# Optimization experiments

Measured on AMD Instinct MI355X. Metric: run time of the kernel, lower is better.

The kernel has to match this reference:

```python
import jax, jax.numpy as jnp
import numpy as np

N_ENTITIES = 100000
N_RELATIONS = 1000
EMBED_DIM = 256
BATCH = 1024


def setup_inputs() -> dict:
    key = jax.random.key(0)
    k1, k2, k3 = jax.random.split(key, 3)
    queries = jax.random.randint(k1, (BATCH, 3), 0, N_RELATIONS, dtype=jnp.int64)
    entity_emb = jax.random.normal(k2, (N_ENTITIES, EMBED_DIM), dtype=jnp.float32)
    relation_emb = jax.random.normal(k3, (N_RELATIONS, EMBED_DIM), dtype=jnp.float32)
    return {"queries": queries, "entity_emb": entity_emb, "relation_emb": relation_emb}


def reference(queries, entity_emb, relation_emb):
    """Score every entity as the tail of each (head, relation, ?) query.

    Original torch code loops over entities computing
      -||E[head] + R[rel] - E[tail]||^2
    per tail. We collapse this into one GEMM via the expansion
      ||hr - E||^2 = ||hr||^2 - 2 hr.E^T + ||E||^2.
    """
    heads = queries[:, 0]
    rels = queries[:, 1]
    hr = entity_emb[heads] + relation_emb[rels]          # [B, D]
    hr_sq = jnp.sum(hr * hr, axis=-1, keepdims=True)      # [B, 1]
    ent_sq = jnp.sum(entity_emb * entity_emb, axis=-1)    # [N]
    cross = jnp.einsum("bd,nd->bn", hr, entity_emb)      # [B, N]
    scores = -(hr_sq - 2.0 * cross + ent_sq[None, :])     # [B, N]
    predictions = jnp.argmax(scores, axis=-1)             # [B]
    return scores, predictions
```

## Files before the change

kernel.cpp:

```cpp
#include <hip/hip_runtime.h>

#define MM 1024
#define NE 100000
#define KD 256
#define NT 782
#define NTILE 1563
#define PSTRIDE 784

typedef __attribute__((ext_vector_type(8))) short bf16x8;
typedef __attribute__((ext_vector_type(4))) float f32x4;
typedef __attribute__((ext_vector_type(4))) short short4v;

#define WS_HRSQ   524288
#define WS_ENTSQ  528384
#define WS_PART   1048576
#define WS_ENTB   8388608
#define WS_NEED   (WS_ENTB + (size_t)NE * KD * 2)

#define AS1 __attribute__((address_space(1)))
#define AS3 __attribute__((address_space(3)))

__device__ __forceinline__ void gld_lds16(const void* g, void* l) {
    __builtin_amdgcn_global_load_lds((const AS1 unsigned int*)g,
                                     (AS3 unsigned int*)l, 16, 0, 0);
}

__device__ __forceinline__ unsigned short f2bf(float f) {
    union { float f; unsigned int u; } v; v.f = f;
    unsigned int u = v.u;
    return (unsigned short)((u + 0x7FFFu + ((u >> 16) & 1u)) >> 16);
}

__device__ __forceinline__ bf16x8 pack8(float4 a, float4 b) {
    bf16x8 t;
    t[0] = (short)f2bf(a.x); t[1] = (short)f2bf(a.y);
    t[2] = (short)f2bf(a.z); t[3] = (short)f2bf(a.w);
    t[4] = (short)f2bf(b.x); t[5] = (short)f2bf(b.y);
    t[6] = (short)f2bf(b.z); t[7] = (short)f2bf(b.w);
    return t;
}

__device__ __forceinline__ unsigned long long packkey(float s, int col) {
    unsigned int u = __float_as_uint(s);
    unsigned int key = u ^ ((unsigned int)((int)u >> 31) | 0x80000000u);
    return ((unsigned long long)key << 32) | (unsigned int)(~col);
}

__global__ __launch_bounds__(64) void prep_kernel(const int* __restrict__ q,
                                                  const float* __restrict__ ent,
                                                  const float* __restrict__ rel,
                                                  unsigned short* __restrict__ hrb,
                                                  float* __restrict__ hrsq) {
    int b = blockIdx.x;
    int lane = threadIdx.x;
    int head = q[b * 3 + 0];
    int r    = q[b * 3 + 1];
    float4 e  = ((const float4*)(ent + (size_t)head * KD))[lane];
    float4 rv = ((const float4*)(rel + (size_t)r * KD))[lane];
    float4 h; h.x = e.x + rv.x; h.y = e.y + rv.y; h.z = e.z + rv.z; h.w = e.w + rv.w;
    short4v hv;
    hv[0] = (short)f2bf(h.x); hv[1] = (short)f2bf(h.y);
    hv[2] = (short)f2bf(h.z); hv[3] = (short)f2bf(h.w);
    *(short4v*)(hrb + (size_t)b * KD + lane * 4) = hv;
    float sq = h.x * h.x + h.y * h.y + h.z * h.z + h.w * h.w;
    #pragma unroll
    for (int off = 32; off > 0; off >>= 1) sq += __shfl_down(sq, off, 64);
    if (lane == 0) hrsq[b] = sq;
}

__global__ __launch_bounds__(256) void conv_entsq_kernel(const float* __restrict__ ent,
                                                         unsigned short* __restrict__ entb,
                                                         float* __restrict__ entsq) {
    int gw   = (blockIdx.x * 256 + threadIdx.x) >> 6;
    int lane = threadIdx.x & 63;
    int row  = gw * 2 + (lane >> 5);
    if (row >= NE) return;
    const float4* src = (const float4*)(ent + (size_t)row * KD) + (lane & 31) * 2;
    float4 a = src[0], b = src[1];
    *(bf16x8*)(entb + (size_t)row * KD + (lane & 31) * 8) = pack8(a, b);
    float s = a.x * a.x + a.y * a.y + a.z * a.z + a.w * a.w
            + b.x * b.x + b.y * b.y + b.z * b.z + b.w * b.w;
    #pragma unroll
    for (int off = 16; off > 0; off >>= 1) s += __shfl_xor(s, off, 64);
    if ((lane & 31) == 0) entsq[row] = s;
}

__global__ __launch_bounds__(256) void entsq_kernel(const float* __restrict__ ent,
                                                    float* __restrict__ entsq) {
    int w = threadIdx.x >> 6, lane = threadIdx.x & 63;
    int n = blockIdx.x * 4 + w;
    if (n >= NE) return;
    float4 v = ((const float4*)(ent + (size_t)n * KD))[lane];
    float s = v.x * v.x + v.y * v.y + v.z * v.z + v.w * v.w;
    #pragma unroll
    for (int off = 32; off > 0; off >>= 1) s += __shfl_down(s, off, 64);
    if (lane == 0) entsq[n] = s;
}

__global__ __launch_bounds__(256, 2) void gemm_v14(const unsigned short* __restrict__ hrb,
                                                   const unsigned short* __restrict__ entb,
                                                   const float* __restrict__ hrsq,
                                                   const float* __restrict__ entsq,
                                                   float* __restrict__ out,
                                                   unsigned long long* __restrict__ part) {
    __shared__ __align__(16) char SMEM[65536];

    const int bid    = blockIdx.x;
    const int qpanel = bid >> 6;
    const int g      = bid & 63;
    const int q0     = qpanel * 128;

    const int tid  = threadIdx.x;
    const int lane = tid & 63;
    const int wid  = tid >> 6;
    const int lr = lane & 15;
    const int lg = lane >> 4;
    const int qw = q0 + wid * 32;

    const int nT = (NTILE - g + 63) >> 6;

    float hq[2]; unsigned qoff[2];
    #pragma unroll
    for (int nn = 0; nn < 2; ++nn) {
        int qq = qw + nn * 16 + lr;
        hq[nn] = hrsq[qq];
        qoff[nn] = (unsigned)qq * (unsigned)NE;
    }
    bf16x8 bq[8][2];
    #pragma unroll
    for (int ks = 0; ks < 8; ++ks)
        #pragma unroll
        for (int nn = 0; nn < 2; ++nn)
            bq[ks][nn] = *(const bf16x8*)(hrb + (size_t)(qw + nn * 16 + lr) * KD
                                          + ks * 32 + lg * 8);

    const char* ebB = (const char*)entb;
    #define STAGE_TILE(T, PAR)                                                  \
    {                                                                           \
        const int e0s_  = (T) * 64;                                            \
        char* dbase_ = SMEM + (PAR) * 32768 + wid * 8192;                       \
        _Pragma("unroll")                                                       \
        for (int si_ = 0; si_ < 8; ++si_) {                                     \
            int L_ = wid * 8192 + si_ * 1024 + lane * 16;                       \
            int row_ = L_ >> 9;                                                 \
            int Gx_ = L_ ^ ((row_ & 7) << 4);                                   \
            int er_ = e0s_ + row_; er_ = er_ < NE ? er_ : (NE - 1);             \
            gld_lds16(ebB + (size_t)er_ * 512 + (Gx_ & 511),                    \
                      dbase_ + si_ * 1024);                                     \
        }                                                                       \
    }

    STAGE_TILE(g, 0);

    float bestf[2]; int bestc[2];
    #pragma unroll
    for (int nn = 0; nn < 2; ++nn) { bestf[nn] = -3.4e38f; bestc[nn] = 0; }

    __syncthreads();

    for (int i = 0; i < nT; ++i) {
        const int t = g + (i << 6);
        const int e0 = t * 64;

        if (i + 1 < nT) STAGE_TILE(t + 64, (i + 1) & 1);

        float4 eqv[4];
        #pragma unroll
        for (int mm = 0; mm < 4; ++mm) {
            int ebq = e0 + mm * 16 + lg * 4;
            ebq = ebq < (NE - 4) ? ebq : (NE - 4);
            eqv[mm] = *(const float4*)(entsq + ebq);
        }

        const char* buf = SMEM + (i & 1) * 32768;
        f32x4 acc[4][2];
        #pragma unroll
        for (int mm = 0; mm < 4; ++mm)
            #pragma unroll
            for (int nn = 0; nn < 2; ++nn)
                acc[mm][nn] = (f32x4){0.f, 0.f, 0.f, 0.f};

        #pragma unroll
        for (int ks = 0; ks < 8; ++ks) {
            bf16x8 af[4];
            #pragma unroll
            for (int mm = 0; mm < 4; ++mm) {
                int r = mm * 16 + lr;
                int byte = r * 512 + ((ks * 64 + lg * 16) ^ ((r & 7) << 4));
                af[mm] = *(const bf16x8*)(buf + byte);
            }
            #pragma unroll
            for (int mm = 0; mm < 4; ++mm)
                #pragma unroll
                for (int nn = 0; nn < 2; ++nn)
                    acc[mm][nn] = __builtin_amdgcn_mfma_f32_16x16x32_bf16(af[mm], bq[ks][nn], acc[mm][nn], 0, 0, 0);
        }

        __syncthreads();

        #pragma unroll
        for (int mm = 0; mm < 4; ++mm) {
            const int eb = e0 + mm * 16 + lg * 4;
            if (eb < NE) {
                const float4 eq = eqv[mm];
                #pragma unroll
                for (int nn = 0; nn < 2; ++nn) {
                    float4 sv;
                    sv.x = 2.0f * acc[mm][nn][0] - hq[nn] - eq.x;
                    sv.y = 2.0f * acc[mm][nn][1] - hq[nn] - eq.y;
                    sv.z = 2.0f * acc[mm][nn][2] - hq[nn] - eq.z;
                    sv.w = 2.0f * acc[mm][nn][3] - hq[nn] - eq.w;
                    *(float4*)(out + qoff[nn] + (unsigned)eb) = sv;
                    if (sv.x > bestf[nn]) { bestf[nn] = sv.x; bestc[nn] = eb; }
                    if (sv.y > bestf[nn]) { bestf[nn] = sv.y; bestc[nn] = eb + 1; }
                    if (sv.z > bestf[nn]) { bestf[nn] = sv.z; bestc[nn] = eb + 2; }
                    if (sv.w > bestf[nn]) { bestf[nn] = sv.w; bestc[nn] = eb + 3; }
                }
            }
        }
    }

    #pragma unroll
    for (int nn = 0; nn < 2; ++nn) {
        unsigned long long best = packkey(bestf[nn], bestc[nn]);
        #pragma unroll
        for (int off = 16; off <= 32; off <<= 1) {
            unsigned long long o =
                (unsigned long long)__shfl_xor((long long)best, off, 64);
            best = (o > best) ? o : best;
        }
        if (lg == 0)
            part[(size_t)(qw + nn * 16 + lr) * PSTRIDE + g] = best;
    }
    #undef STAGE_TILE
}

__global__ __launch_bounds__(256, 3) void gemm_direct_f32(const unsigned short* __restrict__ hrb,
                                                          const float* __restrict__ entf,
                                                          const float* __restrict__ hrsq,
                                                          const float* __restrict__ entsq,
                                                          float* __restrict__ out,
                                                          unsigned long long* __restrict__ part) {
    __shared__ unsigned long long lds_best[2][128];
    const int bid  = blockIdx.x;
    const int wgid = (bid & 7) * NT + (bid >> 3);
    const int mt = wgid & 7, nt = wgid >> 3;
    const int m0 = mt * 128, n0 = nt * 128;
    const int tid  = threadIdx.x;
    const int lane = tid & 63;
    const int wid  = tid >> 6;
    const int wr = wid >> 1, wc = wid & 1;
    const int lr = lane & 15;
    const int lk = (lane >> 4) * 8;

    const unsigned short* aP[4];
    const float*          bPf[4];
    int  cg[4];
    bool cv[4];
    #pragma unroll
    for (int i = 0; i < 4; ++i) {
        int ar = m0 + wr * 64 + i * 16 + lr;
        aP[i] = hrb + (size_t)ar * KD + lk;
        int nr = n0 + wc * 64 + i * 16 + lr;
        cg[i] = nr; cv[i] = nr < NE;
        bPf[i] = entf + (size_t)(cv[i] ? nr : 0) * KD + lk;
    }

    f32x4 acc[4][4];
    #pragma unroll
    for (int m = 0; m < 4; ++m)
        #pragma unroll
        for (int n = 0; n < 4; ++n)
            acc[m][n] = (f32x4){0.f, 0.f, 0.f, 0.f};

    #pragma unroll
    for (int ks = 0; ks < KD / 32; ++ks) {
        bf16x8 af[4], bfr[4];
        #pragma unroll
        for (int i = 0; i < 4; ++i)
            af[i] = *(const bf16x8*)(aP[i] + ks * 32);
        #pragma unroll
        for (int i = 0; i < 4; ++i) {
            const float4* p = (const float4*)(bPf[i] + ks * 32);
            bfr[i] = pack8(p[0], p[1]);
        }
        #pragma unroll
        for (int m = 0; m < 4; ++m)
            #pragma unroll
            for (int n = 0; n < 4; ++n)
                acc[m][n] = __builtin_amdgcn_mfma_f32_16x16x32_bf16(af[m], bfr[n], acc[m][n], 0, 0, 0);
    }

    float eq[4];
    #pragma unroll
    for (int n = 0; n < 4; ++n) eq[n] = cv[n] ? entsq[cg[n]] : 0.f;

    unsigned long long rowbest[4][4];
    #pragma unroll
    for (int m = 0; m < 4; ++m) {
        #pragma unroll
        for (int j = 0; j < 4; ++j) {
            int rg = m0 + wr * 64 + m * 16 + ((lane >> 4) << 2) + j;
            float hqv = hrsq[rg];
            size_t ro = (size_t)rg * NE;
            unsigned long long best = 0ull;
            #pragma unroll
            for (int n = 0; n < 4; ++n) {
                if (cv[n]) {
                    float s = 2.0f * acc[m][n][j] - hqv - eq[n];
                    out[ro + cg[n]] = s;
                    unsigned long long k64 = packkey(s, cg[n]);
                    best = (k64 > best) ? k64 : best;
                }
            }
            #pragma unroll
            for (int off = 8; off > 0; off >>= 1) {
                unsigned long long o =
                    (unsigned long long)__shfl_xor((long long)best, off, 16);
                best = (o > best) ? o : best;
            }
            rowbest[m][j] = best;
        }
    }
    if (lr == 0) {
        int gg = lane >> 4;
        #pragma unroll
        for (int m = 0; m < 4; ++m)
            #pragma unroll
            for (int j = 0; j < 4; ++j)
                lds_best[wc][wr * 64 + m * 16 + gg * 4 + j] = rowbest[m][j];
    }
    __syncthreads();
    if (tid < 128) {
        unsigned long long a = lds_best[0][tid];
        unsigned long long b = lds_best[1][tid];
        unsigned long long best = a > b ? a : b;
        part[(size_t)(m0 + tid) * PSTRIDE + nt] = best;
    }
}

__global__ __launch_bounds__(256) void reduce_kernel(const unsigned long long* __restrict__ part,
                                                     float* __restrict__ pred, int np) {
    __shared__ unsigned long long sb[256];
    int row = blockIdx.x;
    int tid = threadIdx.x;
    const unsigned long long* base = part + (size_t)row * PSTRIDE;
    unsigned long long best = 0ull;
    for (int i = tid; i < np; i += 256) {
        unsigned long long v = base[i];
        best = v > best ? v : best;
    }
    sb[tid] = best;
    __syncthreads();
    #pragma unroll
    for (int s = 128; s > 0; s >>= 1) {
        if (tid < s) {
            unsigned long long o = sb[tid + s];
            if (o > sb[tid]) sb[tid] = o;
        }
        __syncthreads();
    }
    if (tid == 0) {
        unsigned int ic = (unsigned int)(sb[0] & 0xFFFFFFFFull);
        pred[row] = (float)(~ic);
    }
}

extern "C" void kernel_launch(void* const* d_in, const int* in_sizes, int n_in,
                              void* d_out, int out_size, void* d_ws, size_t ws_size,
                              hipStream_t stream) {
    const int*   q   = (const int*)d_in[0];
    const float* ent = (const float*)d_in[1];
    const float* rel = (const float*)d_in[2];
    float* out = (float*)d_out;
    char*  ws  = (char*)d_ws;

    unsigned short*     hrb   = (unsigned short*)ws;
    float*              hrsq  = (float*)(ws + WS_HRSQ);
    float*              entsq = (float*)(ws + WS_ENTSQ);
    unsigned long long* part  = (unsigned long long*)(ws + WS_PART);
    unsigned short*     entb  = (unsigned short*)(ws + WS_ENTB);
    float* pred = out + (size_t)MM * NE;

    prep_kernel<<<MM, 64, 0, stream>>>(q, ent, rel, hrb, hrsq);

    if (ws_size >= WS_NEED) {
        conv_entsq_kernel<<<12500, 256, 0, stream>>>(ent, entb, entsq);
        gemm_v14<<<8 * 64, 256, 0, stream>>>(hrb, entb, hrsq, entsq, out, part);
        reduce_kernel<<<MM, 256, 0, stream>>>(part, pred, 64);
    } else {
        entsq_kernel<<<(NE + 3) / 4, 256, 0, stream>>>(ent, entsq);
        gemm_direct_f32<<<8 * NT, 256, 0, stream>>>(hrb, ent, hrsq, entsq, out, part);
        reduce_kernel<<<MM, 256, 0, stream>>>(part, pred, NT);
    }
}
```

Before: 165.7 us.

## Split GEMM workgroup into 8 waves each owning 16 queries

The main bf16 GEMM kernel now launches 512 threads (8 waves) per block instead of 256. Each wave handles 16 query rows instead of 32, which halves the per-wave accumulators, B fragments and argmax state. Tile staging is spread across 8 waves with 4 loads each. The aim is more waves in flight per CU to hide the latency of LDS reads and output stores. The cost is that each LDS A-fragment read now feeds half as many MFMAs, and the launch-bounds occupancy request is raised to 4.

```diff
diff --git a/kernel.cpp b/kernel.cpp
--- a/kernel.cpp
+++ b/kernel.cpp
@@ -97,7 +97,7 @@
     if (lane == 0) entsq[n] = s;
 }
 
-__global__ __launch_bounds__(256, 2) void gemm_v14(const unsigned short* __restrict__ hrb,
+__global__ __launch_bounds__(512, 4) void gemm_v15(const unsigned short* __restrict__ hrb,
                                                    const unsigned short* __restrict__ entb,
                                                    const float* __restrict__ hrsq,
                                                    const float* __restrict__ entsq,
@@ -115,33 +115,25 @@
     const int wid  = tid >> 6;
     const int lr = lane & 15;
     const int lg = lane >> 4;
-    const int qw = q0 + wid * 32;
+    const int qq = q0 + wid * 16 + lr;
 
     const int nT = (NTILE - g + 63) >> 6;
 
-    float hq[2]; unsigned qoff[2];
-    #pragma unroll
-    for (int nn = 0; nn < 2; ++nn) {
-        int qq = qw + nn * 16 + lr;
-        hq[nn] = hrsq[qq];
-        qoff[nn] = (unsigned)qq * (unsigned)NE;
-    }
-    bf16x8 bq[8][2];
+    const float hq = hrsq[qq];
+    const unsigned qoff = (unsigned)qq * (unsigned)NE;
+    bf16x8 bq[8];
     #pragma unroll
     for (int ks = 0; ks < 8; ++ks)
-        #pragma unroll
-        for (int nn = 0; nn < 2; ++nn)
-            bq[ks][nn] = *(const bf16x8*)(hrb + (size_t)(qw + nn * 16 + lr) * KD
-                                          + ks * 32 + lg * 8);
+        bq[ks] = *(const bf16x8*)(hrb + (size_t)qq * KD + ks * 32 + lg * 8);
 
     const char* ebB = (const char*)entb;
     #define STAGE_TILE(T, PAR)                                                  \
     {                                                                           \
         const int e0s_  = (T) * 64;                                            \
-        char* dbase_ = SMEM + (PAR) * 32768 + wid * 8192;                       \
+        char* dbase_ = SMEM + (PAR) * 32768 + wid * 4096;                       \
         _Pragma("unroll")                                                       \
-        for (int si_ = 0; si_ < 8; ++si_) {                                     \
-            int L_ = wid * 8192 + si_ * 1024 + lane * 16;                       \
+        for (int si_ = 0; si_ < 4; ++si_) {                                     \
+            int L_ = wid * 4096 + si_ * 1024 + lane * 16;                       \
             int row_ = L_ >> 9;                                                 \
             int Gx_ = L_ ^ ((row_ & 7) << 4);                                   \
             int er_ = e0s_ + row_; er_ = er_ < NE ? er_ : (NE - 1);             \
@@ -152,9 +144,8 @@
 
     STAGE_TILE(g, 0);
 
-    float bestf[2]; int bestc[2];
-    #pragma unroll
-    for (int nn = 0; nn < 2; ++nn) { bestf[nn] = -3.4e38f; bestc[nn] = 0; }
+    float bestf = -3.4e38f;
+    int   bestc = 0;
 
     __syncthreads();
 
@@ -173,12 +164,9 @@
         }
 
         const char* buf = SMEM + (i & 1) * 32768;
-        f32x4 acc[4][2];
-        #pragma unroll
-        for (int mm = 0; mm < 4; ++mm)
-            #pragma unroll
-            for (int nn = 0; nn < 2; ++nn)
-                acc[mm][nn] = (f32x4){0.f, 0.f, 0.f, 0.f};
+        f32x4 acc[4];
+        #pragma unroll
+        for (int mm = 0; mm < 4; ++mm) acc[mm] = (f32x4){0.f, 0.f, 0.f, 0.f};
 
         #pragma unroll
         for (int ks = 0; ks < 8; ++ks) {
@@ -191,9 +179,7 @@
             }
             #pragma unroll
             for (int mm = 0; mm < 4; ++mm)
-                #pragma unroll
-                for (int nn = 0; nn < 2; ++nn)
-                    acc[mm][nn] = __builtin_amdgcn_mfma_f32_16x16x32_bf16(af[mm], bq[ks][nn], acc[mm][nn], 0, 0, 0);
+                acc[mm] = __builtin_amdgcn_mfma_f32_16x16x32_bf16(af[mm], bq[ks], acc[mm], 0, 0, 0);
         }
 
         __syncthreads();
@@ -203,26 +189,22 @@
             const int eb = e0 + mm * 16 + lg * 4;
             if (eb < NE) {
                 const float4 eq = eqv[mm];
-                #pragma unroll
-                for (int nn = 0; nn < 2; ++nn) {
-                    float4 sv;
-                    sv.x = 2.0f * acc[mm][nn][0] - hq[nn] - eq.x;
-                    sv.y = 2.0f * acc[mm][nn][1] - hq[nn] - eq.y;
-                    sv.z = 2.0f * acc[mm][nn][2] - hq[nn] - eq.z;
-                    sv.w = 2.0f * acc[mm][nn][3] - hq[nn] - eq.w;
-                    *(float4*)(out + qoff[nn] + (unsigned)eb) = sv;
-                    if (sv.x > bestf[nn]) { bestf[nn] = sv.x; bestc[nn] = eb; }
-                    if (sv.y > bestf[nn]) { bestf[nn] = sv.y; bestc[nn] = eb + 1; }
-                    if (sv.z > bestf[nn]) { bestf[nn] = sv.z; bestc[nn] = eb + 2; }
-                    if (sv.w > bestf[nn]) { bestf[nn] = sv.w; bestc[nn] = eb + 3; }
-                }
+                float4 sv;
+                sv.x = 2.0f * acc[mm][0] - hq - eq.x;
+                sv.y = 2.0f * acc[mm][1] - hq - eq.y;
+                sv.z = 2.0f * acc[mm][2] - hq - eq.z;
+                sv.w = 2.0f * acc[mm][3] - hq - eq.w;
+                *(float4*)(out + qoff + (unsigned)eb) = sv;
+                if (sv.x > bestf) { bestf = sv.x; bestc = eb; }
+                if (sv.y > bestf) { bestf = sv.y; bestc = eb + 1; }
+                if (sv.z > bestf) { bestf = sv.z; bestc = eb + 2; }
+                if (sv.w > bestf) { bestf = sv.w; bestc = eb + 3; }
             }
         }
     }
 
-    #pragma unroll
-    for (int nn = 0; nn < 2; ++nn) {
-        unsigned long long best = packkey(bestf[nn], bestc[nn]);
+    {
+        unsigned long long best = packkey(bestf, bestc);
         #pragma unroll
         for (int off = 16; off <= 32; off <<= 1) {
             unsigned long long o =
@@ -230,7 +212,7 @@
             best = (o > best) ? o : best;
         }
         if (lg == 0)
-            part[(size_t)(qw + nn * 16 + lr) * PSTRIDE + g] = best;
+            part[(size_t)qq * PSTRIDE + g] = best;
     }
     #undef STAGE_TILE
 }
@@ -386,7 +368,7 @@
 
     if (ws_size >= WS_NEED) {
         conv_entsq_kernel<<<12500, 256, 0, stream>>>(ent, entb, entsq);
-        gemm_v14<<<8 * 64, 256, 0, stream>>>(hrb, entb, hrsq, entsq, out, part);
+        gemm_v15<<<8 * 64, 512, 0, stream>>>(hrb, entb, hrsq, entsq, out, part);
         reduce_kernel<<<MM, 256, 0, stream>>>(part, pred, 64);
     } else {
         entsq_kernel<<<(NE + 3) / 4, 256, 0, stream>>>(ent, entsq);
```

New measurement: 180.4 us. 8.9% more time.
